# Kernel optimization log

Hardware: AMD Instinct MI355X
Metric: run time of the kernel (lower is better)

Reference implementation:

```python
import jax, jax.numpy as jnp
import numpy as np

N, E = 50000, 800000
DIN, H, R, HEADS, DH, OUT = 256, 128, 8, 8, 16, 3  # DH = H // HEADS


def setup_inputs() -> dict:
    key = jax.random.key(0)
    ks = jax.random.split(key, 16)
    g = lambda k, shape, fan: jax.random.normal(k, shape, jnp.float32) * np.float32(np.sqrt(2.0 / fan))
    return {
        'x': jax.random.normal(ks[0], (N, DIN), jnp.float32),
        'edge_index': jax.random.randint(ks[1], (2, E), 0, N, jnp.int32),
        'edge_type': jax.random.randint(ks[2], (E,), 0, R, jnp.int32),
        'Wp': g(ks[3], (DIN, H), DIN), 'bp': jnp.zeros((H,), jnp.float32),
        'W1': g(ks[4], (R, H, H), H), 'root1': g(ks[5], (H, H), H), 'b1': jnp.zeros((H,), jnp.float32),
        'W2': g(ks[6], (R, H, H), H), 'root2': g(ks[7], (H, H), H), 'b2': jnp.zeros((H,), jnp.float32),
        'Wg': g(ks[8], (H, HEADS * DH), H), 'att': g(ks[9], (1, HEADS, 2 * DH), 2 * DH),
        'bg': jnp.zeros((HEADS * DH,), jnp.float32),
        'Wf': g(ks[10], (H, OUT), H), 'bf': jnp.zeros((OUT,), jnp.float32),
    }


def _rgcn(h, src, tgt, etype, W, root, b):
    # h: [N,H]; per-relation: mean-aggregate W_r @ h_src over edges of type r
    n = h.shape[0]
    h_src = h[src]                                   # [E,H]
    out = h @ root
    for r in range(R):
        mask = (etype == r)
        msg = jnp.where(mask[:, None], h_src @ W[r], 0.0)          # [E,H]
        agg = jax.ops.segment_sum(msg, tgt, num_segments=n)        # [N,H]
        deg = jax.ops.segment_sum(mask.astype(h.dtype), tgt, num_segments=n)
        out = out + agg / jnp.clip(deg, 1.0)[:, None]
    return out + b


def _gat(h, src, tgt, Wg, att, bg, negative_slope=0.2):
    n = h.shape[0]
    z = (h @ Wg).reshape(n, HEADS, DH)               # [N,heads,dh]
    z_src, z_tgt = z[src], z[tgt]                    # [E,heads,dh]
    alpha = (z_src * att[:, :, :DH]).sum(-1) + (z_tgt * att[:, :, DH:]).sum(-1)  # [E,heads]
    alpha = jax.nn.leaky_relu(alpha, negative_slope)
    amax = jax.ops.segment_max(alpha, tgt, num_segments=n)         # [N,heads]
    ex = jnp.exp(alpha - amax[tgt])
    denom = jnp.clip(jax.ops.segment_sum(ex, tgt, num_segments=n), 1e-16)
    alpha = ex / denom[tgt]
    out = jax.ops.segment_sum(z_src * alpha[:, :, None], tgt, num_segments=n)  # [N,heads,dh]
    return out.reshape(n, HEADS * DH) + bg


def reference(x, edge_index, edge_type, Wp, bp, W1, root1, b1, W2, root2, b2, Wg, att, bg, Wf, bf):
    src, tgt = edge_index[0], edge_index[1]
    h = x @ Wp + bp
    h = jax.nn.relu(_rgcn(h, src, tgt, edge_type, W1, root1, b1))
    h = jax.nn.relu(_rgcn(h, src, tgt, edge_type, W2, root2, b2))
    h = _gat(h, src, tgt, Wg, att, bg)
    logits = h @ Wf + bf
    return jax.nn.log_softmax(logits, axis=-1)
```

## Files before the change

kernel.cpp:

```cpp
#include <hip/hip_runtime.h>
#include <math.h>

#define NN      50000
#define EE      800000
#define DIN     256
#define HF      128
#define RR      8
#define NHEADS  8
#define DHH     16
#define OUTC    3
#define M2      (NN * RR)
#define NB2     ((M2 + 255) / 256)
#define CH2     ((NB2 + 255) / 256)

static inline int cdiv(long long a, int b) { return (int)((a + b - 1) / b); }

typedef __attribute__((ext_vector_type(8))) short short8;
typedef __attribute__((ext_vector_type(4))) float f32x4;

__device__ inline float bf2f(unsigned short u) {
    return __uint_as_float(((unsigned)u) << 16);
}
__device__ inline unsigned short f2bf(float f) {
    unsigned u = __float_as_uint(f);
    u += 0x7fffu + ((u >> 16) & 1u);
    return (unsigned short)(u >> 16);
}

__global__ __launch_bounds__(256) void prep_weights(const float* __restrict__ Wp,
                                                    const float* __restrict__ W1,
                                                    const float* __restrict__ root1,
                                                    const float* __restrict__ W2,
                                                    const float* __restrict__ root2,
                                                    const float* __restrict__ Wg,
                                                    unsigned short* __restrict__ Wtp_hi,
                                                    unsigned short* __restrict__ Wtp_lo,
                                                    unsigned short* __restrict__ Wt1_hi,
                                                    unsigned short* __restrict__ Wt1_lo,
                                                    unsigned short* __restrict__ Wt2_hi,
                                                    unsigned short* __restrict__ Wt2_lo,
                                                    unsigned short* __restrict__ Wtg_hi,
                                                    unsigned short* __restrict__ Wtg_lo) {
    int i = blockIdx.x * 256 + threadIdx.x;
    if (i >= 344064) return;
    const float* src; unsigned short *dh, *dl; int k0, ldk, base;
    if (i < 32768)       { src = Wp;    dh = Wtp_hi; dl = Wtp_lo; k0 = 0;    ldk = 256;  base = 0; }
    else if (i < 163840) { src = W1;    dh = Wt1_hi; dl = Wt1_lo; k0 = 0;    ldk = 1152; base = 32768; }
    else if (i < 180224) { src = root1; dh = Wt1_hi; dl = Wt1_lo; k0 = 1024; ldk = 1152; base = 163840; }
    else if (i < 311296) { src = W2;    dh = Wt2_hi; dl = Wt2_lo; k0 = 0;    ldk = 1152; base = 180224; }
    else if (i < 327680) { src = root2; dh = Wt2_hi; dl = Wt2_lo; k0 = 1024; ldk = 1152; base = 311296; }
    else                 { src = Wg;    dh = Wtg_hi; dl = Wtg_lo; k0 = 0;    ldk = 128;  base = 327680; }
    int j = i - base;
    int k = j >> 7, n = j & 127;
    float f = src[(size_t)k * 128 + n];
    unsigned short hi = f2bf(f);
    unsigned short lo = f2bf(f - bf2f(hi));
    dh[(size_t)n * ldk + k0 + k] = hi;
    dl[(size_t)n * ldk + k0 + k] = lo;
}

__global__ __launch_bounds__(256) void count2_kernel(const int* __restrict__ tgt,
                                                     const int* __restrict__ et,
                                                     int* __restrict__ cnt2) {
    int i = blockIdx.x * 256 + threadIdx.x;
    if (i < EE) atomicAdd(&cnt2[tgt[i] * RR + et[i]], 1);
}

__global__ __launch_bounds__(256) void scan1_kernel(const int* __restrict__ cnt,
                                                    int* __restrict__ bsum, int n) {
    __shared__ int s[256];
    int t = threadIdx.x;
    int i = blockIdx.x * 256 + t;
    s[t] = (i < n) ? cnt[i] : 0;
    __syncthreads();
    for (int off = 128; off > 0; off >>= 1) {
        if (t < off) s[t] += s[t + off];
        __syncthreads();
    }
    if (t == 0) bsum[blockIdx.x] = s[0];
}

__global__ __launch_bounds__(256) void scan2_kernel(const int* __restrict__ bsum,
                                                    int* __restrict__ bbase,
                                                    int* __restrict__ tail,
                                                    int nb, int ch) {
    __shared__ int s[256];
    int t = threadIdx.x;
    int beg = t * ch;
    int end = beg + ch; if (end > nb) end = nb;
    int sum = 0;
    for (int i = beg; i < end; i++) sum += bsum[i];
    s[t] = sum;
    __syncthreads();
    for (int off = 1; off < 256; off <<= 1) {
        int u = (t >= off) ? s[t - off] : 0;
        __syncthreads();
        s[t] += u;
        __syncthreads();
    }
    int run = s[t] - sum;
    for (int i = beg; i < end; i++) {
        bbase[i] = run;
        run += bsum[i];
    }
    if (t == 255) *tail = s[255];
}

__global__ __launch_bounds__(256) void scan3_kernel(const int* __restrict__ cnt,
                                                    const int* __restrict__ bbase,
                                                    int* __restrict__ rowptr,
                                                    int* __restrict__ cursor, int n) {
    __shared__ int s[256];
    int t = threadIdx.x;
    int i = blockIdx.x * 256 + t;
    int v = (i < n) ? cnt[i] : 0;
    s[t] = v;
    __syncthreads();
    for (int off = 1; off < 256; off <<= 1) {
        int u = (t >= off) ? s[t - off] : 0;
        __syncthreads();
        s[t] += u;
        __syncthreads();
    }
    if (i < n) {
        int e = bbase[blockIdx.x] + s[t] - v;
        rowptr[i] = e;
        cursor[i] = e;
    }
}

__global__ __launch_bounds__(256) void fill2_kernel(const int* __restrict__ src,
                                                    const int* __restrict__ tgt,
                                                    const int* __restrict__ et,
                                                    int* __restrict__ cursor2,
                                                    int* __restrict__ csr_src2) {
    int e = blockIdx.x * 256 + threadIdx.x;
    if (e >= EE) return;
    int pos = atomicAdd(&cursor2[tgt[e] * RR + et[e]], 1);
    csr_src2[pos] = src[e];
}

#define BK 32
#define APAD 36

template <bool SPLITA, bool ACC, bool BIAS, bool RELU, bool BF16OUT>
__global__ __launch_bounds__(256) void gemm_mfma(const void* __restrict__ Av, int lda,
                                                 const unsigned short* __restrict__ Bthi,
                                                 const unsigned short* __restrict__ Btlo, int ldk,
                                                 float* __restrict__ C,
                                                 unsigned short* __restrict__ Cb,
                                                 const float* __restrict__ bias,
                                                 int M, int K) {
    __shared__ unsigned short Ah[128 * APAD];
    __shared__ unsigned short Al[(SPLITA ? 128 : 1) * APAD];
    __shared__ unsigned short Bh[128 * APAD];
    __shared__ unsigned short Bl[128 * APAD];
    const int tid  = threadIdx.x;
    const int m0   = blockIdx.x * 128;
    const int w    = tid >> 6;
    const int lane = tid & 63;
    const int lrow = lane & 15;
    const int q    = lane >> 4;

    f32x4 acc[2][8];
#pragma unroll
    for (int t = 0; t < 2; t++)
#pragma unroll
        for (int c = 0; c < 8; c++) acc[t][c] = (f32x4){0.f, 0.f, 0.f, 0.f};

    const int srow  = tid >> 1;
    const int spart = (tid & 1) * 16;

    for (int k0 = 0; k0 < K; k0 += BK) {
        if (SPLITA) {
            const float* A = (const float*)Av;
            int gm = m0 + srow;
            float va[16];
            if (gm < M) {
                const float* ap = &A[(size_t)gm * lda + k0 + spart];
#pragma unroll
                for (int j = 0; j < 4; j++) {
                    float4 v = *reinterpret_cast<const float4*>(ap + j * 4);
                    va[j * 4 + 0] = v.x; va[j * 4 + 1] = v.y; va[j * 4 + 2] = v.z; va[j * 4 + 3] = v.w;
                }
            } else {
#pragma unroll
                for (int j = 0; j < 16; j++) va[j] = 0.f;
            }
            unsigned hw[8], lw[8];
#pragma unroll
            for (int j = 0; j < 8; j++) {
                unsigned short h0 = f2bf(va[2 * j]);
                unsigned short h1 = f2bf(va[2 * j + 1]);
                unsigned short l0 = f2bf(va[2 * j] - bf2f(h0));
                unsigned short l1 = f2bf(va[2 * j + 1] - bf2f(h1));
                hw[j] = (unsigned)h0 | ((unsigned)h1 << 16);
                lw[j] = (unsigned)l0 | ((unsigned)l1 << 16);
            }
            *reinterpret_cast<uint4*>(&Ah[srow * APAD + spart])     = make_uint4(hw[0], hw[1], hw[2], hw[3]);
            *reinterpret_cast<uint4*>(&Ah[srow * APAD + spart + 8]) = make_uint4(hw[4], hw[5], hw[6], hw[7]);
            *reinterpret_cast<uint4*>(&Al[srow * APAD + spart])     = make_uint4(lw[0], lw[1], lw[2], lw[3]);
            *reinterpret_cast<uint4*>(&Al[srow * APAD + spart + 8]) = make_uint4(lw[4], lw[5], lw[6], lw[7]);
        } else {
            const unsigned short* A = (const unsigned short*)Av;
            int gm = m0 + srow;
            uint4 v  = make_uint4(0u, 0u, 0u, 0u);
            uint4 v2 = make_uint4(0u, 0u, 0u, 0u);
            if (gm < M) {
                const unsigned short* ap = &A[(size_t)gm * lda + k0 + spart];
                v  = *reinterpret_cast<const uint4*>(ap);
                v2 = *reinterpret_cast<const uint4*>(ap + 8);
            }
            *reinterpret_cast<uint4*>(&Ah[srow * APAD + spart])     = v;
            *reinterpret_cast<uint4*>(&Ah[srow * APAD + spart + 8]) = v2;
        }
        {
            const unsigned short* bh = &Bthi[(size_t)srow * ldk + k0 + spart];
            const unsigned short* bl = &Btlo[(size_t)srow * ldk + k0 + spart];
            *reinterpret_cast<uint4*>(&Bh[srow * APAD + spart])     = *reinterpret_cast<const uint4*>(bh);
            *reinterpret_cast<uint4*>(&Bh[srow * APAD + spart + 8]) = *reinterpret_cast<const uint4*>(bh + 8);
            *reinterpret_cast<uint4*>(&Bl[srow * APAD + spart])     = *reinterpret_cast<const uint4*>(bl);
            *reinterpret_cast<uint4*>(&Bl[srow * APAD + spart + 8]) = *reinterpret_cast<const uint4*>(bl + 8);
        }
        __syncthreads();

        short8 ah[2], al[2];
#pragma unroll
        for (int t = 0; t < 2; t++) {
            ah[t] = *reinterpret_cast<const short8*>(&Ah[(w * 32 + t * 16 + lrow) * APAD + q * 8]);
            if (SPLITA)
                al[t] = *reinterpret_cast<const short8*>(&Al[(w * 32 + t * 16 + lrow) * APAD + q * 8]);
        }
#pragma unroll
        for (int c = 0; c < 8; c++) {
            short8 bh = *reinterpret_cast<const short8*>(&Bh[(c * 16 + lrow) * APAD + q * 8]);
            short8 bl = *reinterpret_cast<const short8*>(&Bl[(c * 16 + lrow) * APAD + q * 8]);
#pragma unroll
            for (int t = 0; t < 2; t++) {
                acc[t][c] = __builtin_amdgcn_mfma_f32_16x16x32_bf16(ah[t], bl, acc[t][c], 0, 0, 0);
                if (SPLITA)
                    acc[t][c] = __builtin_amdgcn_mfma_f32_16x16x32_bf16(al[t], bh, acc[t][c], 0, 0, 0);
                acc[t][c] = __builtin_amdgcn_mfma_f32_16x16x32_bf16(ah[t], bh, acc[t][c], 0, 0, 0);
            }
        }
        __syncthreads();
    }

#pragma unroll
    for (int t = 0; t < 2; t++) {
#pragma unroll
        for (int r = 0; r < 4; r++) {
            int gm = m0 + w * 32 + t * 16 + q * 4 + r;
            if (gm >= M) continue;
#pragma unroll
            for (int c = 0; c < 8; c++) {
                int gn = c * 16 + lrow;
                float v = acc[t][c][r];
                if (BIAS) v += bias[gn];
                if (ACC)  v += C[(size_t)gm * HF + gn];
                if (RELU) v = fmaxf(v, 0.f);
                C[(size_t)gm * HF + gn] = v;
                if (BF16OUT) Cb[(size_t)gm * HF + gn] = f2bf(v);
            }
        }
    }
}

__global__ __launch_bounds__(256) void gemm_rgcn(const unsigned short* __restrict__ aggb,
                                                 const float* __restrict__ hin,
                                                 const unsigned short* __restrict__ Bthi,
                                                 const unsigned short* __restrict__ Btlo,
                                                 float* __restrict__ hout,
                                                 unsigned short* __restrict__ hbout,
                                                 const float* __restrict__ bias, int M) {
    const int LDK = (RR + 1) * HF;
    __shared__ unsigned short Ah[128 * APAD];
    __shared__ unsigned short Al[128 * APAD];
    __shared__ unsigned short Bh[128 * APAD];
    __shared__ unsigned short Bl[128 * APAD];
    const int tid  = threadIdx.x;
    const int m0   = blockIdx.x * 128;
    const int w    = tid >> 6;
    const int lane = tid & 63;
    const int lrow = lane & 15;
    const int q    = lane >> 4;

    f32x4 acc[2][8];
#pragma unroll
    for (int t = 0; t < 2; t++)
#pragma unroll
        for (int c = 0; c < 8; c++) acc[t][c] = (f32x4){0.f, 0.f, 0.f, 0.f};

    const int srow  = tid >> 1;
    const int spart = (tid & 1) * 16;

    for (int k0 = 0; k0 < RR * HF; k0 += BK) {
        {
            int gm = m0 + srow;
            uint4 v  = make_uint4(0u, 0u, 0u, 0u);
            uint4 v2 = make_uint4(0u, 0u, 0u, 0u);
            if (gm < M) {
                const unsigned short* ap = &aggb[(size_t)gm * (RR * HF) + k0 + spart];
                v  = *reinterpret_cast<const uint4*>(ap);
                v2 = *reinterpret_cast<const uint4*>(ap + 8);
            }
            *reinterpret_cast<uint4*>(&Ah[srow * APAD + spart])     = v;
            *reinterpret_cast<uint4*>(&Ah[srow * APAD + spart + 8]) = v2;
        }
        {
            const unsigned short* bh = &Bthi[(size_t)srow * LDK + k0 + spart];
            const unsigned short* bl = &Btlo[(size_t)srow * LDK + k0 + spart];
            *reinterpret_cast<uint4*>(&Bh[srow * APAD + spart])     = *reinterpret_cast<const uint4*>(bh);
            *reinterpret_cast<uint4*>(&Bh[srow * APAD + spart + 8]) = *reinterpret_cast<const uint4*>(bh + 8);
            *reinterpret_cast<uint4*>(&Bl[srow * APAD + spart])     = *reinterpret_cast<const uint4*>(bl);
            *reinterpret_cast<uint4*>(&Bl[srow * APAD + spart + 8]) = *reinterpret_cast<const uint4*>(bl + 8);
        }
        __syncthreads();
        short8 ah[2];
#pragma unroll
        for (int t = 0; t < 2; t++)
            ah[t] = *reinterpret_cast<const short8*>(&Ah[(w * 32 + t * 16 + lrow) * APAD + q * 8]);
#pragma unroll
        for (int c = 0; c < 8; c++) {
            short8 bh = *reinterpret_cast<const short8*>(&Bh[(c * 16 + lrow) * APAD + q * 8]);
            short8 bl = *reinterpret_cast<const short8*>(&Bl[(c * 16 + lrow) * APAD + q * 8]);
#pragma unroll
            for (int t = 0; t < 2; t++) {
                acc[t][c] = __builtin_amdgcn_mfma_f32_16x16x32_bf16(ah[t], bl, acc[t][c], 0, 0, 0);
                acc[t][c] = __builtin_amdgcn_mfma_f32_16x16x32_bf16(ah[t], bh, acc[t][c], 0, 0, 0);
            }
        }
        __syncthreads();
    }

    for (int k0 = 0; k0 < HF; k0 += BK) {
        {
            int gm = m0 + srow;
            float va[16];
            if (gm < M) {
                const float* ap = &hin[(size_t)gm * HF + k0 + spart];
#pragma unroll
                for (int j = 0; j < 4; j++) {
                    float4 v = *reinterpret_cast<const float4*>(ap + j * 4);
                    va[j * 4 + 0] = v.x; va[j * 4 + 1] = v.y; va[j * 4 + 2] = v.z; va[j * 4 + 3] = v.w;
                }
            } else {
#pragma unroll
                for (int j = 0; j < 16; j++) va[j] = 0.f;
            }
            unsigned hw[8], lw[8];
#pragma unroll
            for (int j = 0; j < 8; j++) {
                unsigned short h0 = f2bf(va[2 * j]);
                unsigned short h1 = f2bf(va[2 * j + 1]);
                unsigned short l0 = f2bf(va[2 * j] - bf2f(h0));
                unsigned short l1 = f2bf(va[2 * j + 1] - bf2f(h1));
                hw[j] = (unsigned)h0 | ((unsigned)h1 << 16);
                lw[j] = (unsigned)l0 | ((unsigned)l1 << 16);
            }
            *reinterpret_cast<uint4*>(&Ah[srow * APAD + spart])     = make_uint4(hw[0], hw[1], hw[2], hw[3]);
            *reinterpret_cast<uint4*>(&Ah[srow * APAD + spart + 8]) = make_uint4(hw[4], hw[5], hw[6], hw[7]);
            *reinterpret_cast<uint4*>(&Al[srow * APAD + spart])     = make_uint4(lw[0], lw[1], lw[2], lw[3]);
            *reinterpret_cast<uint4*>(&Al[srow * APAD + spart + 8]) = make_uint4(lw[4], lw[5], lw[6], lw[7]);
        }
        {
            const unsigned short* bh = &Bthi[(size_t)srow * LDK + RR * HF + k0 + spart];
            const unsigned short* bl = &Btlo[(size_t)srow * LDK + RR * HF + k0 + spart];
            *reinterpret_cast<uint4*>(&Bh[srow * APAD + spart])     = *reinterpret_cast<const uint4*>(bh);
            *reinterpret_cast<uint4*>(&Bh[srow * APAD + spart + 8]) = *reinterpret_cast<const uint4*>(bh + 8);
            *reinterpret_cast<uint4*>(&Bl[srow * APAD + spart])     = *reinterpret_cast<const uint4*>(bl);
            *reinterpret_cast<uint4*>(&Bl[srow * APAD + spart + 8]) = *reinterpret_cast<const uint4*>(bl + 8);
        }
        __syncthreads();
        short8 ah[2], al[2];
#pragma unroll
        for (int t = 0; t < 2; t++) {
            ah[t] = *reinterpret_cast<const short8*>(&Ah[(w * 32 + t * 16 + lrow) * APAD + q * 8]);
            al[t] = *reinterpret_cast<const short8*>(&Al[(w * 32 + t * 16 + lrow) * APAD + q * 8]);
        }
#pragma unroll
        for (int c = 0; c < 8; c++) {
            short8 bh = *reinterpret_cast<const short8*>(&Bh[(c * 16 + lrow) * APAD + q * 8]);
            short8 bl = *reinterpret_cast<const short8*>(&Bl[(c * 16 + lrow) * APAD + q * 8]);
#pragma unroll
            for (int t = 0; t < 2; t++) {
                acc[t][c] = __builtin_amdgcn_mfma_f32_16x16x32_bf16(ah[t], bl, acc[t][c], 0, 0, 0);
                acc[t][c] = __builtin_amdgcn_mfma_f32_16x16x32_bf16(al[t], bh, acc[t][c], 0, 0, 0);
                acc[t][c] = __builtin_amdgcn_mfma_f32_16x16x32_bf16(ah[t], bh, acc[t][c], 0, 0, 0);
            }
        }
        __syncthreads();
    }

#pragma unroll
    for (int t = 0; t < 2; t++) {
#pragma unroll
        for (int r = 0; r < 4; r++) {
            int gm = m0 + w * 32 + t * 16 + q * 4 + r;
            if (gm >= M) continue;
#pragma unroll
            for (int c = 0; c < 8; c++) {
                int gn = c * 16 + lrow;
                float v = fmaxf(acc[t][c][r] + bias[gn], 0.f);
                hout[(size_t)gm * HF + gn] = v;
                hbout[(size_t)gm * HF + gn] = f2bf(v);
            }
        }
    }
}

__global__ __launch_bounds__(256) void gemm_z(const float* __restrict__ hin,
                                              const unsigned short* __restrict__ Bthi,
                                              const unsigned short* __restrict__ Btlo,
                                              const float* __restrict__ att,
                                              unsigned short* __restrict__ zb,
                                              float* __restrict__ a_src,
                                              float* __restrict__ a_tgt, int M) {
    __shared__ unsigned short Ah[128 * APAD];
    __shared__ unsigned short Al[128 * APAD];
    __shared__ unsigned short Bh[128 * APAD];
    __shared__ unsigned short Bl[128 * APAD];
    const int tid  = threadIdx.x;
    const int m0   = blockIdx.x * 128;
    const int w    = tid >> 6;
    const int lane = tid & 63;
    const int lrow = lane & 15;
    const int q    = lane >> 4;

    f32x4 acc[2][8];
#pragma unroll
    for (int t = 0; t < 2; t++)
#pragma unroll
        for (int c = 0; c < 8; c++) acc[t][c] = (f32x4){0.f, 0.f, 0.f, 0.f};

    const int srow  = tid >> 1;
    const int spart = (tid & 1) * 16;

    for (int k0 = 0; k0 < HF; k0 += BK) {
        {
            int gm = m0 + srow;
            float va[16];
            if (gm < M) {
                const float* ap = &hin[(size_t)gm * HF + k0 + spart];
#pragma unroll
                for (int j = 0; j < 4; j++) {
                    float4 v = *reinterpret_cast<const float4*>(ap + j * 4);
                    va[j * 4 + 0] = v.x; va[j * 4 + 1] = v.y; va[j * 4 + 2] = v.z; va[j * 4 + 3] = v.w;
                }
            } else {
#pragma unroll
                for (int j = 0; j < 16; j++) va[j] = 0.f;
            }
            unsigned hw[8], lw[8];
#pragma unroll
            for (int j = 0; j < 8; j++) {
                unsigned short h0 = f2bf(va[2 * j]);
                unsigned short h1 = f2bf(va[2 * j + 1]);
                unsigned short l0 = f2bf(va[2 * j] - bf2f(h0));
                unsigned short l1 = f2bf(va[2 * j + 1] - bf2f(h1));
                hw[j] = (unsigned)h0 | ((unsigned)h1 << 16);
                lw[j] = (unsigned)l0 | ((unsigned)l1 << 16);
            }
            *reinterpret_cast<uint4*>(&Ah[srow * APAD + spart])     = make_uint4(hw[0], hw[1], hw[2], hw[3]);
            *reinterpret_cast<uint4*>(&Ah[srow * APAD + spart + 8]) = make_uint4(hw[4], hw[5], hw[6], hw[7]);
            *reinterpret_cast<uint4*>(&Al[srow * APAD + spart])     = make_uint4(lw[0], lw[1], lw[2], lw[3]);
            *reinterpret_cast<uint4*>(&Al[srow * APAD + spart + 8]) = make_uint4(lw[4], lw[5], lw[6], lw[7]);
        }
        {
            const unsigned short* bh = &Bthi[(size_t)srow * HF + k0 + spart];
            const unsigned short* bl = &Btlo[(size_t)srow * HF + k0 + spart];
            *reinterpret_cast<uint4*>(&Bh[srow * APAD + spart])     = *reinterpret_cast<const uint4*>(bh);
            *reinterpret_cast<uint4*>(&Bh[srow * APAD + spart + 8]) = *reinterpret_cast<const uint4*>(bh + 8);
            *reinterpret_cast<uint4*>(&Bl[srow * APAD + spart])     = *reinterpret_cast<const uint4*>(bl);
            *reinterpret_cast<uint4*>(&Bl[srow * APAD + spart + 8]) = *reinterpret_cast<const uint4*>(bl + 8);
        }
        __syncthreads();
        short8 ah[2], al[2];
#pragma unroll
        for (int t = 0; t < 2; t++) {
            ah[t] = *reinterpret_cast<const short8*>(&Ah[(w * 32 + t * 16 + lrow) * APAD + q * 8]);
            al[t] = *reinterpret_cast<const short8*>(&Al[(w * 32 + t * 16 + lrow) * APAD + q * 8]);
        }
#pragma unroll
        for (int c = 0; c < 8; c++) {
            short8 bh = *reinterpret_cast<const short8*>(&Bh[(c * 16 + lrow) * APAD + q * 8]);
            short8 bl = *reinterpret_cast<const short8*>(&Bl[(c * 16 + lrow) * APAD + q * 8]);
#pragma unroll
            for (int t = 0; t < 2; t++) {
                acc[t][c] = __builtin_amdgcn_mfma_f32_16x16x32_bf16(ah[t], bl, acc[t][c], 0, 0, 0);
                acc[t][c] = __builtin_amdgcn_mfma_f32_16x16x32_bf16(al[t], bh, acc[t][c], 0, 0, 0);
                acc[t][c] = __builtin_amdgcn_mfma_f32_16x16x32_bf16(ah[t], bh, acc[t][c], 0, 0, 0);
            }
        }
        __syncthreads();
    }

    float att_s[8], att_t[8];
#pragma unroll
    for (int c = 0; c < 8; c++) {
        att_s[c] = att[c * 32 + lrow];
        att_t[c] = att[c * 32 + 16 + lrow];
    }

#pragma unroll
    for (int t = 0; t < 2; t++) {
#pragma unroll
        for (int r = 0; r < 4; r++) {
            int gm = m0 + w * 32 + t * 16 + q * 4 + r;
            if (gm >= M) continue;
#pragma unroll
            for (int c = 0; c < 8; c++) {
                int gn = c * 16 + lrow;
                float v = acc[t][c][r];
                zb[(size_t)gm * HF + gn] = f2bf(v);
                float ps = v * att_s[c];
                float pt = v * att_t[c];
#pragma unroll
                for (int off = 1; off < 16; off <<= 1) {
                    ps += __shfl_xor(ps, off);
                    pt += __shfl_xor(pt, off);
                }
                if (lrow == 0) {
                    a_src[(size_t)gm * NHEADS + c] = ps;
                    a_tgt[(size_t)gm * NHEADS + c] = pt;
                }
            }
        }
    }
}

__device__ inline void acc8(float* a, uint4 v) {
    a[0] += bf2f((unsigned short)(v.x & 0xffffu));
    a[1] += bf2f((unsigned short)(v.x >> 16));
    a[2] += bf2f((unsigned short)(v.y & 0xffffu));
    a[3] += bf2f((unsigned short)(v.y >> 16));
    a[4] += bf2f((unsigned short)(v.z & 0xffffu));
    a[5] += bf2f((unsigned short)(v.z >> 16));
    a[6] += bf2f((unsigned short)(v.w & 0xffffu));
    a[7] += bf2f((unsigned short)(v.w >> 16));
}

__global__ __launch_bounds__(256) void rgcn_agg_sorted(const unsigned short* __restrict__ hb,
                                                       const int* __restrict__ rowptr2,
                                                       const int* __restrict__ csr_src2,
                                                       unsigned short* __restrict__ agg) {
    int w = (blockIdx.x * 256 + threadIdx.x) >> 6;
    if (w >= NN) return;
    int lane = threadIdx.x & 63;
    int r    = lane >> 3;
    int cg   = (lane & 7) * 16;
    int b8   = w * RR;

    int rp  = rowptr2[b8 + (lane < 9 ? lane : 8)];
    int beg = __shfl(rp, r);
    int end = __shfl(rp, r + 1);

    float a[16];
#pragma unroll
    for (int j = 0; j < 16; j++) a[j] = 0.f;

    int e = beg;
    for (; e + 1 < end; e += 2) {
        int s0 = csr_src2[e];
        int s1 = csr_src2[e + 1];
        const uint4* p0 = reinterpret_cast<const uint4*>(&hb[(size_t)s0 * HF + cg]);
        const uint4* p1 = reinterpret_cast<const uint4*>(&hb[(size_t)s1 * HF + cg]);
        uint4 v00 = p0[0];
        uint4 v01 = p0[1];
        uint4 v10 = p1[0];
        uint4 v11 = p1[1];
        acc8(a,     v00);
        acc8(a + 8, v01);
        acc8(a,     v10);
        acc8(a + 8, v11);
    }
    if (e < end) {
        int s0 = csr_src2[e];
        const uint4* p0 = reinterpret_cast<const uint4*>(&hb[(size_t)s0 * HF + cg]);
        uint4 v00 = p0[0];
        uint4 v01 = p0[1];
        acc8(a,     v00);
        acc8(a + 8, v01);
    }

    int n = end - beg;
    float inv = 1.f / (float)(n > 1 ? n : 1);
    unsigned ow[8];
#pragma unroll
    for (int j = 0; j < 8; j++) {
        ow[j] = (unsigned)f2bf(a[2 * j] * inv) | ((unsigned)f2bf(a[2 * j + 1] * inv) << 16);
    }
    unsigned short* o = &agg[(size_t)w * (RR * HF) + r * HF + cg];
    *reinterpret_cast<uint4*>(o)     = make_uint4(ow[0], ow[1], ow[2], ow[3]);
    *reinterpret_cast<uint4*>(o + 8) = make_uint4(ow[4], ow[5], ow[6], ow[7]);
}

__global__ __launch_bounds__(256) void gat_kernel(const int* __restrict__ rowptr2,
                                                  const int* __restrict__ csr_src2,
                                                  const float* __restrict__ a_src,
                                                  const float* __restrict__ a_tgt,
                                                  const unsigned short* __restrict__ zb,
                                                  const float* __restrict__ bg,
                                                  const float* __restrict__ Wf,
                                                  const float* __restrict__ bf,
                                                  float* __restrict__ out) {
    int w = (blockIdx.x * 256 + threadIdx.x) >> 6;
    if (w >= NN) return;
    int lane = threadIdx.x & 63;
    int beg = rowptr2[w * RR], end = rowptr2[w * RR + RR];

    int hdA = lane & 7;
    int e8  = lane >> 3;
    float atA = a_tgt[w * NHEADS + hdA];
    float m = -1e30f;
    for (int e = beg + e8; e < end; e += 8) {
        int s = csr_src2[e];
        float a = a_src[s * NHEADS + hdA] + atA;
        a = a > 0.f ? a : 0.2f * a;
        m = fmaxf(m, a);
    }
    m = fmaxf(m, __shfl_xor(m, 8));
    m = fmaxf(m, __shfl_xor(m, 16));
    m = fmaxf(m, __shfl_xor(m, 32));

    int hd = lane >> 3;
    int c0 = lane * 2;
    float mB = __shfl(m, hd);
    float at = __shfl(atA, hd);
    float l0 = 0.f, l1 = 0.f;
    float ax0 = 0.f, ay0 = 0.f, ax1 = 0.f, ay1 = 0.f;
    int e = beg;
    for (; e + 1 < end; e += 2) {
        int s0 = csr_src2[e], s1 = csr_src2[e + 1];
        float a0 = a_src[s0 * NHEADS + hd] + at;
        float a1 = a_src[s1 * NHEADS + hd] + at;
        a0 = a0 > 0.f ? a0 : 0.2f * a0;
        a1 = a1 > 0.f ? a1 : 0.2f * a1;
        float w0 = __expf(a0 - mB);
        float w1 = __expf(a1 - mB);
        unsigned z0 = *reinterpret_cast<const unsigned*>(&zb[(size_t)s0 * HF + c0]);
        unsigned z1 = *reinterpret_cast<const unsigned*>(&zb[(size_t)s1 * HF + c0]);
        l0 += w0; l1 += w1;
        ax0 += bf2f((unsigned short)(z0 & 0xffffu)) * w0;
        ay0 += bf2f((unsigned short)(z0 >> 16)) * w0;
        ax1 += bf2f((unsigned short)(z1 & 0xffffu)) * w1;
        ay1 += bf2f((unsigned short)(z1 >> 16)) * w1;
    }
    if (e < end) {
        int s0 = csr_src2[e];
        float a0 = a_src[s0 * NHEADS + hd] + at;
        a0 = a0 > 0.f ? a0 : 0.2f * a0;
        float w0 = __expf(a0 - mB);
        unsigned z0 = *reinterpret_cast<const unsigned*>(&zb[(size_t)s0 * HF + c0]);
        l0 += w0;
        ax0 += bf2f((unsigned short)(z0 & 0xffffu)) * w0;
        ay0 += bf2f((unsigned short)(z0 >> 16)) * w0;
    }
    float l = l0 + l1;
    float ax = ax0 + ax1, ay = ay0 + ay1;

    float inv = 1.f / fmaxf(l, 1e-16f);
    float vx = ax * inv + bg[c0];
    float vy = ay * inv + bg[c0 + 1];

    float p0 = vx * Wf[c0 * 3 + 0] + vy * Wf[(c0 + 1) * 3 + 0];
    float p1 = vx * Wf[c0 * 3 + 1] + vy * Wf[(c0 + 1) * 3 + 1];
    float p2 = vx * Wf[c0 * 3 + 2] + vy * Wf[(c0 + 1) * 3 + 2];
#pragma unroll
    for (int off = 32; off > 0; off >>= 1) {
        p0 += __shfl_xor(p0, off);
        p1 += __shfl_xor(p1, off);
        p2 += __shfl_xor(p2, off);
    }
    if (lane == 0) {
        float l0v = p0 + bf[0], l1v = p1 + bf[1], l2v = p2 + bf[2];
        float mm = fmaxf(l0v, fmaxf(l1v, l2v));
        float lse = mm + logf(expf(l0v - mm) + expf(l1v - mm) + expf(l2v - mm));
        out[(size_t)w * 3 + 0] = l0v - lse;
        out[(size_t)w * 3 + 1] = l1v - lse;
        out[(size_t)w * 3 + 2] = l2v - lse;
    }
}

extern "C" void kernel_launch(void* const* d_in, const int* in_sizes, int n_in,
                              void* d_out, int out_size, void* d_ws, size_t ws_size,
                              hipStream_t stream) {
    const float* x     = (const float*)d_in[0];
    const int*   ei    = (const int*)d_in[1];
    const int*   etype = (const int*)d_in[2];
    const float* Wp    = (const float*)d_in[3];
    const float* bp    = (const float*)d_in[4];
    const float* W1    = (const float*)d_in[5];
    const float* root1 = (const float*)d_in[6];
    const float* b1    = (const float*)d_in[7];
    const float* W2    = (const float*)d_in[8];
    const float* root2 = (const float*)d_in[9];
    const float* b2    = (const float*)d_in[10];
    const float* Wg    = (const float*)d_in[11];
    const float* att   = (const float*)d_in[12];
    const float* bg    = (const float*)d_in[13];
    const float* Wf    = (const float*)d_in[14];
    const float* bf    = (const float*)d_in[15];
    (void)in_sizes; (void)n_in; (void)out_size; (void)ws_size;

    const int* srcv = ei;
    const int* tgtv = ei + EE;

    char* base = (char*)d_ws;
    unsigned short* aggb = (unsigned short*)(base + 0);
    int* cnt2    = (int*)(base + 96000000);
    int* cursor2 = (int*)(base + 98000000);
    int* bsum2   = (int*)(base + 99700000);
    int* bbase2  = (int*)(base + 99800000);
    unsigned short* zb = (unsigned short*)(base + 0);
    float* a_src = (float*)(base + 12800000);
    float* a_tgt = (float*)(base + 14400000);
    float* h1    = (float*)(base + 102400000);
    float* h2    = (float*)(base + 128000000);
    unsigned short* h1b = (unsigned short*)(base + 153600000);
    unsigned short* h2b = (unsigned short*)(base + 166400000);
    int* csr_src2 = (int*)(base + 179200000);
    int* rowptr2  = (int*)(base + 182400000);
    unsigned short* Wtp_hi = (unsigned short*)(base + 184000016);
    unsigned short* Wtp_lo = (unsigned short*)(base + 184065552);
    unsigned short* Wt1_hi = (unsigned short*)(base + 184131088);
    unsigned short* Wt1_lo = (unsigned short*)(base + 184426000);
    unsigned short* Wt2_hi = (unsigned short*)(base + 184720912);
    unsigned short* Wt2_lo = (unsigned short*)(base + 185015824);
    unsigned short* Wtg_hi = (unsigned short*)(base + 185310736);
    unsigned short* Wtg_lo = (unsigned short*)(base + 185343504);

    prep_weights<<<cdiv(344064, 256), 256, 0, stream>>>(
        Wp, W1, root1, W2, root2, Wg,
        Wtp_hi, Wtp_lo, Wt1_hi, Wt1_lo, Wt2_hi, Wt2_lo, Wtg_hi, Wtg_lo);

    hipMemsetAsync(cnt2, 0, (size_t)M2 * 4, stream);
    count2_kernel<<<cdiv(EE, 256), 256, 0, stream>>>(tgtv, etype, cnt2);
    scan1_kernel<<<NB2, 256, 0, stream>>>(cnt2, bsum2, M2);
    scan2_kernel<<<1, 256, 0, stream>>>(bsum2, bbase2, &rowptr2[M2], NB2, CH2);
    scan3_kernel<<<NB2, 256, 0, stream>>>(cnt2, bbase2, rowptr2, cursor2, M2);
    fill2_kernel<<<cdiv(EE, 256), 256, 0, stream>>>(srcv, tgtv, etype, cursor2, csr_src2);

    const int ggrid  = cdiv(NN, 128);
    const int nwgrid = cdiv(NN, 4);

    gemm_mfma<true, false, true, false, true><<<ggrid, 256, 0, stream>>>(
        x, DIN, Wtp_hi, Wtp_lo, DIN, h1, h1b, bp, NN, DIN);

    rgcn_agg_sorted<<<nwgrid, 256, 0, stream>>>(h1b, rowptr2, csr_src2, aggb);
    gemm_rgcn<<<ggrid, 256, 0, stream>>>(aggb, h1, Wt1_hi, Wt1_lo, h2, h2b, b1, NN);

    rgcn_agg_sorted<<<nwgrid, 256, 0, stream>>>(h2b, rowptr2, csr_src2, aggb);
    gemm_rgcn<<<ggrid, 256, 0, stream>>>(aggb, h2, Wt2_hi, Wt2_lo, h1, h1b, b2, NN);

    gemm_z<<<ggrid, 256, 0, stream>>>(h1, Wtg_hi, Wtg_lo, att, zb, a_src, a_tgt, NN);
    gat_kernel<<<nwgrid, 256, 0, stream>>>(rowptr2, csr_src2, a_src, a_tgt, zb, bg, Wf, bf, (float*)d_out);
}
```

Measured before the change: 525.7 us.

## Compute GAT edge weights once per edge-head and broadcast via shuffles in aggregation

In the fused GAT aggregation kernel, each lane now computes the leaky-relu/exp weight for one (edge, head) pair in a batch of 8 edges, then broadcasts the weights and source indices through shuffles. The two half-waves each process alternate edges with 4 features per lane (8-byte loads) and are combined with a cross-half shuffle at the end. Each weight is no longer recomputed by all 8 lanes that share a head, and the gathers become wider. The cost is extra shuffle traffic and masked lanes on the tail when the degree is not a multiple of 8.

After: 509.1 us. 1.03x faster.

```diff
diff --git a/kernel.cpp b/kernel.cpp
--- a/kernel.cpp
+++ b/kernel.cpp
@@ -623,51 +623,57 @@
     m = fmaxf(m, __shfl_xor(m, 16));
     m = fmaxf(m, __shfl_xor(m, 32));
 
-    int hd = lane >> 3;
-    int c0 = lane * 2;
-    float mB = __shfl(m, hd);
-    float at = __shfl(atA, hd);
-    float l0 = 0.f, l1 = 0.f;
-    float ax0 = 0.f, ay0 = 0.f, ax1 = 0.f, ay1 = 0.f;
-    int e = beg;
-    for (; e + 1 < end; e += 2) {
-        int s0 = csr_src2[e], s1 = csr_src2[e + 1];
-        float a0 = a_src[s0 * NHEADS + hd] + at;
-        float a1 = a_src[s1 * NHEADS + hd] + at;
-        a0 = a0 > 0.f ? a0 : 0.2f * a0;
-        a1 = a1 > 0.f ? a1 : 0.2f * a1;
-        float w0 = __expf(a0 - mB);
-        float w1 = __expf(a1 - mB);
-        unsigned z0 = *reinterpret_cast<const unsigned*>(&zb[(size_t)s0 * HF + c0]);
-        unsigned z1 = *reinterpret_cast<const unsigned*>(&zb[(size_t)s1 * HF + c0]);
-        l0 += w0; l1 += w1;
-        ax0 += bf2f((unsigned short)(z0 & 0xffffu)) * w0;
-        ay0 += bf2f((unsigned short)(z0 >> 16)) * w0;
-        ax1 += bf2f((unsigned short)(z1 & 0xffffu)) * w1;
-        ay1 += bf2f((unsigned short)(z1 >> 16)) * w1;
-    }
-    if (e < end) {
-        int s0 = csr_src2[e];
-        float a0 = a_src[s0 * NHEADS + hd] + at;
-        a0 = a0 > 0.f ? a0 : 0.2f * a0;
-        float w0 = __expf(a0 - mB);
-        unsigned z0 = *reinterpret_cast<const unsigned*>(&zb[(size_t)s0 * HF + c0]);
-        l0 += w0;
-        ax0 += bf2f((unsigned short)(z0 & 0xffffu)) * w0;
-        ay0 += bf2f((unsigned short)(z0 >> 16)) * w0;
-    }
-    float l = l0 + l1;
-    float ax = ax0 + ax1, ay = ay0 + ay1;
+    int half = lane >> 5;
+    int l32  = lane & 31;
+    int hd   = l32 >> 2;
+    int c0   = l32 * 4;
+
+    float l = 0.f;
+    float ax0 = 0.f, ax1 = 0.f, ax2 = 0.f, ax3 = 0.f;
+
+    for (int e0 = beg; e0 < end; e0 += 8) {
+        int eA = e0 + e8;
+        float wA = 0.f;
+        int   sA = 0;
+        if (eA < end) {
+            sA = csr_src2[eA];
+            float a = a_src[sA * NHEADS + hdA] + atA;
+            a = a > 0.f ? a : 0.2f * a;
+            wA = __expf(a - m);
+        }
+#pragma unroll
+        for (int j = 0; j < 4; j++) {
+            int idx  = (2 * j + half) * 8 + hd;
+            float wv = __shfl(wA, idx);
+            int   sv = __shfl(sA, idx);
+            uint2 z = *reinterpret_cast<const uint2*>(&zb[(size_t)sv * HF + c0]);
+            l   += wv;
+            ax0 += bf2f((unsigned short)(z.x & 0xffffu)) * wv;
+            ax1 += bf2f((unsigned short)(z.x >> 16)) * wv;
+            ax2 += bf2f((unsigned short)(z.y & 0xffffu)) * wv;
+            ax3 += bf2f((unsigned short)(z.y >> 16)) * wv;
+        }
+    }
+    l   += __shfl_xor(l, 32);
+    ax0 += __shfl_xor(ax0, 32);
+    ax1 += __shfl_xor(ax1, 32);
+    ax2 += __shfl_xor(ax2, 32);
+    ax3 += __shfl_xor(ax3, 32);
 
     float inv = 1.f / fmaxf(l, 1e-16f);
-    float vx = ax * inv + bg[c0];
-    float vy = ay * inv + bg[c0 + 1];
-
-    float p0 = vx * Wf[c0 * 3 + 0] + vy * Wf[(c0 + 1) * 3 + 0];
-    float p1 = vx * Wf[c0 * 3 + 1] + vy * Wf[(c0 + 1) * 3 + 1];
-    float p2 = vx * Wf[c0 * 3 + 2] + vy * Wf[(c0 + 1) * 3 + 2];
-#pragma unroll
-    for (int off = 32; off > 0; off >>= 1) {
+    float v0 = ax0 * inv + bg[c0];
+    float v1 = ax1 * inv + bg[c0 + 1];
+    float v2 = ax2 * inv + bg[c0 + 2];
+    float v3 = ax3 * inv + bg[c0 + 3];
+
+    float p0 = v0 * Wf[c0 * 3 + 0] + v1 * Wf[(c0 + 1) * 3 + 0]
+             + v2 * Wf[(c0 + 2) * 3 + 0] + v3 * Wf[(c0 + 3) * 3 + 0];
+    float p1 = v0 * Wf[c0 * 3 + 1] + v1 * Wf[(c0 + 1) * 3 + 1]
+             + v2 * Wf[(c0 + 2) * 3 + 1] + v3 * Wf[(c0 + 3) * 3 + 1];
+    float p2 = v0 * Wf[c0 * 3 + 2] + v1 * Wf[(c0 + 1) * 3 + 2]
+             + v2 * Wf[(c0 + 2) * 3 + 2] + v3 * Wf[(c0 + 3) * 3 + 2];
+#pragma unroll
+    for (int off = 16; off > 0; off >>= 1) {
         p0 += __shfl_xor(p0, off);
         p1 += __shfl_xor(p1, off);
         p2 += __shfl_xor(p2, off);
```
